# Kernel tuning notes

Hardware: AMD Instinct MI355X
Metric: run time of the kernel (lower is better)

Reference implementation:

```python
import jax, jax.numpy as jnp
import numpy as np

T, B, E, H = 256, 8, 512, 32
EXP = 512            # number of expanded (periodic-image) keys
SMOOTH = 20.0        # smooth_factor


def setup_inputs() -> dict:
    key = jax.random.key(0)
    ks = jax.random.split(key, 12)
    s = 1.0 / np.sqrt(E)
    return {
        "query": jax.random.normal(ks[0], (T, B, E), dtype=jnp.float32),
        "outcell_index": jax.random.randint(ks[1], (B, EXP), 0, T),
        "expand_mask": jax.random.bernoulli(ks[2], 0.1, (B, EXP)),
        "key_padding_mask": jax.random.bernoulli(ks[3], 0.1, (B, T)),
        "local_attention_weight": jax.random.uniform(ks[4], (B, T, T + EXP), dtype=jnp.float32),
        "Wq": jax.random.normal(ks[5], (E, E), dtype=jnp.float32) * s,
        "bq": jnp.zeros((E,), dtype=jnp.float32),
        "Wk": jax.random.normal(ks[6], (E, E), dtype=jnp.float32) * s,   # k_bias=False
        "Wv": jax.random.normal(ks[7], (E, E), dtype=jnp.float32) * s,
        "bv": jnp.zeros((E,), dtype=jnp.float32),
        "Wo": jax.random.normal(ks[8], (E, E), dtype=jnp.float32) * s,
        "bo": jnp.zeros((E,), dtype=jnp.float32),
    }


def reference(query, outcell_index, expand_mask, key_padding_mask,
              local_attention_weight, Wq, bq, Wk, Wv, bv, Wo, bo):
    t, b, e = query.shape
    hd = e // H
    # QKV projections (torch Linear: y = x @ W.T + b)
    q = jnp.einsum('tbe,fe->tbf', query, Wq) + bq
    k = jnp.einsum('tbe,fe->tbf', query, Wk)          # no k bias
    v = jnp.einsum('tbe,fe->tbf', query, Wv) + bv
    # PBC gather-expand K/V along the time axis
    oc = outcell_index.T[:, :, None]                  # [EXP, B, 1]
    k = jnp.concatenate([k, jnp.take_along_axis(k, oc, axis=0)], axis=0)  # [S,B,E]
    v = jnp.concatenate([v, jnp.take_along_axis(v, oc, axis=0)], axis=0)
    s_len = k.shape[0]
    # [len, B, E] -> [B, H, len, hd]
    qh = q.reshape(t, b, H, hd).transpose(1, 2, 0, 3)
    kh = k.reshape(s_len, b, H, hd).transpose(1, 2, 0, 3)
    vh = v.reshape(s_len, b, H, hd).transpose(1, 2, 0, 3)
    # NOTE: forward() never applies self.scaling in this path (faithful)
    scores = jnp.einsum('bhtd,bhsd->bhts', qh, kh)    # [B,H,T,S]
    law = local_attention_weight[:, None]             # [B,1,T,S]
    scores = (scores + SMOOTH) * law - SMOOTH         # smooth softmax
    kpm = jnp.concatenate([key_padding_mask, expand_mask], axis=1)  # [B,S]
    scores = jnp.where(kpm[:, None, None, :], -jnp.inf, scores)
    probs = jax.nn.softmax(scores, axis=-1)
    probs = probs * law                               # post-softmax reweight
    attn = jnp.einsum('bhts,bhsd->bhtd', probs, vh)   # [B,H,T,hd]
    attn = attn.transpose(2, 0, 1, 3).reshape(t, b, e)
    return jnp.einsum('tbe,fe->tbf', attn, Wo) + bo
```

## Files before the change

kernel.cpp:

```cpp
#include <hip/hip_runtime.h>
#include <stdint.h>

#define T_ 256
#define B_ 8
#define E_ 512
#define H_ 32
#define HD_ 16
#define EXP_ 512
#define S_ 768
#define M_ 2048
#define SMOOTH_ 20.0f
#define PSTR 36
#define VSTR 800
#define OSTR 20

typedef __attribute__((ext_vector_type(8)))  short bf16x8;
typedef __attribute__((ext_vector_type(4)))  float f32x4;
typedef __attribute__((ext_vector_type(16))) float f32x16;

__device__ __forceinline__ unsigned int pk2(float a, float b)
{
    unsigned int ua = __float_as_uint(a);
    ua = ua + 0x7FFFu + ((ua >> 16) & 1u);
    unsigned int ub = __float_as_uint(b);
    ub = ub + 0x7FFFu + ((ub >> 16) & 1u);
    return (ua >> 16) | (ub & 0xFFFF0000u);
}
__device__ __forceinline__ ushort bf1(float a)
{
    unsigned int u = __float_as_uint(a);
    u = u + 0x7FFFu + ((u >> 16) & 1u);
    return (ushort)(u >> 16);
}

union U16 { uint4 u; bf16x8 v; };

__global__ __launch_bounds__(256)
void conv_kernel(const float* __restrict__ X,
                 const float* __restrict__ Wq, const float* __restrict__ Wk,
                 const float* __restrict__ Wv, const float* __restrict__ Wo,
                 ushort* __restrict__ Xb, ushort* __restrict__ Wb)
{
    const int seg = blockIdx.x >> 6;
    const int blk = blockIdx.x & 63;
    const float* src;
    ushort* dst;
    if (seg < 4) { src = X + (size_t)seg * 262144; dst = Xb + (size_t)seg * 262144; }
    else {
        const float* ws_[4] = {Wq, Wk, Wv, Wo};
        src = ws_[seg - 4];
        dst = Wb + (size_t)(seg - 4) * 262144;
    }
    const int base = blk * 4096 + threadIdx.x * 16;
    float4 f0 = *(const float4*)&src[base + 0];
    float4 f1 = *(const float4*)&src[base + 4];
    float4 f2 = *(const float4*)&src[base + 8];
    float4 f3 = *(const float4*)&src[base + 12];
    *(uint4*)&dst[base + 0] = make_uint4(pk2(f0.x, f0.y), pk2(f0.z, f0.w),
                                         pk2(f1.x, f1.y), pk2(f1.z, f1.w));
    *(uint4*)&dst[base + 8] = make_uint4(pk2(f2.x, f2.y), pk2(f2.z, f2.w),
                                         pk2(f3.x, f3.y), pk2(f3.z, f3.w));
}

__device__ __forceinline__ void mfma_gemm_body_bf(const ushort* __restrict__ X,
                                                  const ushort* __restrict__ W,
                                                  int m0, int n0,
                                                  f32x4 acc[2][2],
                                                  ushort* As, ushort* Bs)
{
    const int tid  = threadIdx.x;
    const int lrow = tid >> 2;
    const int kq   = tid & 3;
    const int l    = tid & 63;
    const int w    = tid >> 6;
    const int wm   = w & 1;
    const int wn   = w >> 1;
    const int lq   = l >> 4;
    const int ln   = l & 15;

    const ushort* Xr = &X[(size_t)(m0 + lrow) * E_ + kq * 16];
    const ushort* Wr = &W[(size_t)(n0 + lrow) * E_ + kq * 16];
    ushort* Aw = &As[lrow * 72 + kq * 16];
    ushort* Bw = &Bs[lrow * 72 + kq * 16];

    for (int k0 = 0; k0 < E_; k0 += 64) {
        uint4 a0 = *(const uint4*)&Xr[k0 + 0];
        uint4 a1 = *(const uint4*)&Xr[k0 + 8];
        uint4 b0 = *(const uint4*)&Wr[k0 + 0];
        uint4 b1 = *(const uint4*)&Wr[k0 + 8];
        __syncthreads();
        *(uint4*)&Aw[0] = a0;
        *(uint4*)&Aw[8] = a1;
        *(uint4*)&Bw[0] = b0;
        *(uint4*)&Bw[8] = b1;
        __syncthreads();
#pragma unroll
        for (int kb = 0; kb < 2; ++kb) {
            bf16x8 af0 = *(const bf16x8*)&As[(32 * wm + ln) * 72 + 32 * kb + lq * 8];
            bf16x8 af1 = *(const bf16x8*)&As[(32 * wm + 16 + ln) * 72 + 32 * kb + lq * 8];
            bf16x8 bf0 = *(const bf16x8*)&Bs[(32 * wn + ln) * 72 + 32 * kb + lq * 8];
            bf16x8 bf1 = *(const bf16x8*)&Bs[(32 * wn + 16 + ln) * 72 + 32 * kb + lq * 8];
            acc[0][0] = __builtin_amdgcn_mfma_f32_16x16x32_bf16(af0, bf0, acc[0][0], 0, 0, 0);
            acc[0][1] = __builtin_amdgcn_mfma_f32_16x16x32_bf16(af0, bf1, acc[0][1], 0, 0, 0);
            acc[1][0] = __builtin_amdgcn_mfma_f32_16x16x32_bf16(af1, bf0, acc[1][0], 0, 0, 0);
            acc[1][1] = __builtin_amdgcn_mfma_f32_16x16x32_bf16(af1, bf1, acc[1][1], 0, 0, 0);
        }
    }
}

__global__ __launch_bounds__(256)
void qkv_gemm(const ushort* __restrict__ Xb, const ushort* __restrict__ Wb,
              const float* __restrict__ bq, const float* __restrict__ bv,
              ushort* __restrict__ Qb, ushort* __restrict__ Kb,
              ushort* __restrict__ VTb)
{
    __shared__ __align__(16) ushort As[64 * 72];
    __shared__ __align__(16) ushort Bs[64 * 72];
    const int z = blockIdx.z;
    const ushort* W    = Wb + (size_t)z * 262144;
    const float*  bias = (z == 0) ? bq : (z == 2 ? bv : nullptr);

    const int m0 = blockIdx.y * 64;
    const int n0 = blockIdx.x * 64;

    f32x4 acc[2][2];
#pragma unroll
    for (int i = 0; i < 2; ++i)
#pragma unroll
        for (int j = 0; j < 2; ++j)
            acc[i][j] = (f32x4){0.f, 0.f, 0.f, 0.f};

    mfma_gemm_body_bf(Xb, W, m0, n0, acc, As, Bs);

    const int l  = threadIdx.x & 63;
    const int w  = threadIdx.x >> 6;
    const int wm = w & 1;
    const int wn = w >> 1;
    const int lq = l >> 4;
    const int ln = l & 15;

#pragma unroll
    for (int j = 0; j < 2; ++j) {
        const int nb = n0 + 32 * wn + 16 * j;
        const int h  = nb >> 4;
        const int d  = ln;
        const float bv_ = bias ? bias[nb + ln] : 0.f;
#pragma unroll
        for (int i = 0; i < 2; ++i) {
#pragma unroll
            for (int r = 0; r < 4; ++r) {
                const int m = m0 + 32 * wm + 16 * i + lq * 4 + r;
                const int t = m >> 3;
                const int b = m & 7;
                const int bh = b * H_ + h;
                const ushort val = bf1(acc[i][j][r] + bv_);
                if (z == 0)      Qb[((size_t)bh * T_ + t) * HD_ + d] = val;
                else if (z == 1) Kb[((size_t)bh * T_ + t) * HD_ + d] = val;
                else             VTb[((size_t)bh * HD_ + d) * T_ + t] = val;
            }
        }
    }
}

__global__ __launch_bounds__(256)
void out_gemm(const ushort* __restrict__ Ab, const ushort* __restrict__ Wob,
              const float* __restrict__ bo, float* __restrict__ dst)
{
    __shared__ __align__(16) ushort As[64 * 72];
    __shared__ __align__(16) ushort Bs[64 * 72];
    const int m0 = blockIdx.y * 64;
    const int n0 = blockIdx.x * 64;

    f32x4 acc[2][2];
#pragma unroll
    for (int i = 0; i < 2; ++i)
#pragma unroll
        for (int j = 0; j < 2; ++j)
            acc[i][j] = (f32x4){0.f, 0.f, 0.f, 0.f};

    mfma_gemm_body_bf(Ab, Wob, m0, n0, acc, As, Bs);

    const int l  = threadIdx.x & 63;
    const int w  = threadIdx.x >> 6;
    const int wm = w & 1;
    const int wn = w >> 1;
    const int lq = l >> 4;
    const int ln = l & 15;

#pragma unroll
    for (int j = 0; j < 2; ++j) {
        const int nb = n0 + 32 * wn + 16 * j;
        const float bo_ = bo[nb + ln];
#pragma unroll
        for (int i = 0; i < 2; ++i) {
#pragma unroll
            for (int r = 0; r < 4; ++r) {
                const int m = m0 + 32 * wm + 16 * i + lq * 4 + r;
                dst[(size_t)m * E_ + nb + ln] = acc[i][j][r] + bo_;
            }
        }
    }
}

__global__ __launch_bounds__(512)
void attn_kernel(const ushort* __restrict__ Qb, const ushort* __restrict__ Kb,
                 const ushort* __restrict__ VTb, const float* __restrict__ LAW,
                 const int* __restrict__ kpm, const int* __restrict__ em,
                 const int* __restrict__ oc, ushort* __restrict__ Ab)
{
    __shared__ __align__(16) ushort Ks[S_ * HD_];
    __shared__ __align__(16) ushort Vt[HD_ * VSTR];
    __shared__ __align__(16) float  msf[S_];
    __shared__ __align__(16) ushort Pb[8][32 * PSTR];

    float* Obuf = (float*)Ks;
    float* Zb   = (float*)Ks + 128 * OSTR;

    const int tid    = threadIdx.x;
    const int blk    = blockIdx.x;
    const int bh     = blk >> 1;
    const int thalf  = blk & 1;
    const int b      = bh >> 5;
    const int h      = bh & 31;

    ((uint4*)Ks)[tid] = ((const uint4*)&Kb[(size_t)bh * T_ * HD_])[tid];
    {
        const int row = tid >> 5, ch = tid & 31;
        *(uint4*)&Vt[row * VSTR + ch * 8] =
            *(const uint4*)&VTb[((size_t)bh * HD_ + row) * T_ + ch * 8];
    }
    {
        const int j   = tid;
        const int src = oc[b * EXP_ + j];
        const uint4* kr = (const uint4*)&Kb[((size_t)bh * T_ + src) * HD_];
        *(uint4*)&Ks[(T_ + j) * HD_ + 0] = kr[0];
        *(uint4*)&Ks[(T_ + j) * HD_ + 8] = kr[1];
#pragma unroll
        for (int d = 0; d < 16; ++d)
            Vt[d * VSTR + T_ + j] = VTb[((size_t)bh * HD_ + d) * T_ + src];
    }
    {
        const int s = tid;
        const int m = (s < T_) ? kpm[b * T_ + s] : em[b * EXP_ + (s - T_)];
        msf[s] = m ? 0.f : 1.f;
        if (tid < 256) {
            const int s2 = 512 + tid;
            msf[s2] = em[b * EXP_ + (s2 - T_)] ? 0.f : 1.f;
        }
    }

    const int w      = tid >> 6;
    const int l      = tid & 63;
    const int tloc   = l & 31;
    const int khalf  = l >> 5;
    const int wt     = w & 3;
    const int sh     = w >> 2;
    const int tglob  = thalf * 128 + wt * 32 + tloc;
    bf16x8 qf = *(const bf16x8*)&Qb[((size_t)bh * T_ + tglob) * HD_ + khalf * 8];

    __syncthreads();

    const f32x16 zero16 = {0.f,0.f,0.f,0.f,0.f,0.f,0.f,0.f,
                           0.f,0.f,0.f,0.f,0.f,0.f,0.f,0.f};
    f32x4 o0 = {0.f, 0.f, 0.f, 0.f};
    f32x4 o1 = {0.f, 0.f, 0.f, 0.f};
    float Z = 0.f;

    const float* lawp = &LAW[((size_t)b * T_ + tglob) * S_];
    ushort* prow = &Pb[w][tloc * PSTR];
    const int tl = l & 15;
    const int kg = l >> 4;

    for (int i = sh * 12; i < sh * 12 + 12; ++i) {
        bf16x8 kf = *(const bf16x8*)&Ks[(i * 32 + tloc) * HD_ + khalf * 8];
        f32x16 sc = __builtin_amdgcn_mfma_f32_32x32x16_bf16(kf, qf, zero16, 0, 0, 0);

#pragma unroll
        for (int qd = 0; qd < 4; ++qd) {
            const int sb = i * 32 + qd * 8 + khalf * 4;
            float4 mf = *(const float4*)&msf[sb];
            float4 lw = *(const float4*)&lawp[sb];
            float e0, e1, e2, e3;
            {
                float x = (sc[qd*4+0] + SMOOTH_) * lw.x - SMOOTH_;
                e0 = mf.x * __expf(x - 50.f);
                x = (sc[qd*4+1] + SMOOTH_) * lw.y - SMOOTH_;
                e1 = mf.y * __expf(x - 50.f);
                x = (sc[qd*4+2] + SMOOTH_) * lw.z - SMOOTH_;
                e2 = mf.z * __expf(x - 50.f);
                x = (sc[qd*4+3] + SMOOTH_) * lw.w - SMOOTH_;
                e3 = mf.w * __expf(x - 50.f);
            }
            Z += (e0 + e1) + (e2 + e3);
            *(uint2*)&prow[qd * 8 + khalf * 4] =
                make_uint2(pk2(e0 * lw.x, e1 * lw.y), pk2(e2 * lw.z, e3 * lw.w));
        }

        bf16x8 vf = *(const bf16x8*)&Vt[tl * VSTR + i * 32 + kg * 8];
        {
            const ushort* pr0 = &Pb[w][(0 * 16 + tl) * PSTR + kg * 8];
            U16 u;
            uint2 a0 = *(const uint2*)pr0;
            uint2 a1 = *(const uint2*)(pr0 + 4);
            u.u = make_uint4(a0.x, a0.y, a1.x, a1.y);
            o0 = __builtin_amdgcn_mfma_f32_16x16x32_bf16(vf, u.v, o0, 0, 0, 0);
            const ushort* pr1 = &Pb[w][(1 * 16 + tl) * PSTR + kg * 8];
            uint2 b0 = *(const uint2*)pr1;
            uint2 b1 = *(const uint2*)(pr1 + 4);
            u.u = make_uint4(b0.x, b0.y, b1.x, b1.y);
            o1 = __builtin_amdgcn_mfma_f32_16x16x32_bf16(vf, u.v, o1, 0, 0, 0);
        }
    }

    Z += __shfl_xor(Z, 32);

    __syncthreads();

    if (sh == 1) {
#pragma unroll
        for (int th = 0; th < 2; ++th) {
            const f32x4 o = th ? o1 : o0;
            *(float4*)&Obuf[((wt * 2 + th) * 16 + tl) * OSTR + kg * 4] =
                make_float4(o[0], o[1], o[2], o[3]);
        }
        if (l < 32) Zb[wt * 32 + tloc] = Z;
    }
    __syncthreads();

    if (sh == 0) {
        const float Ztot = Z + Zb[wt * 32 + tloc];
#pragma unroll
        for (int th = 0; th < 2; ++th) {
            const float Zt  = __shfl(Ztot, th * 16 + tl);
            const float inv = (Zt > 0.f) ? 1.f / Zt : 0.f;
            float4 po = *(const float4*)&Obuf[((wt * 2 + th) * 16 + tl) * OSTR + kg * 4];
            const f32x4 o = th ? o1 : o0;
            const int t = thalf * 128 + wt * 32 + th * 16 + tl;
            float ov[4] = {o[0] + po.x, o[1] + po.y, o[2] + po.z, o[3] + po.w};
#pragma unroll
            for (int r = 0; r < 4; ++r) {
                const int d = kg * 4 + r;
                Ab[((size_t)t * B_ + b) * E_ + h * HD_ + d] = bf1(ov[r] * inv);
            }
        }
    }
}

extern "C" void kernel_launch(void* const* d_in, const int* in_sizes, int n_in,
                              void* d_out, int out_size, void* d_ws, size_t ws_size,
                              hipStream_t stream)
{
    const float* query = (const float*)d_in[0];
    const int*   oc    = (const int*)d_in[1];
    const int*   em    = (const int*)d_in[2];
    const int*   kpm   = (const int*)d_in[3];
    const float* law   = (const float*)d_in[4];
    const float* Wq    = (const float*)d_in[5];
    const float* bq    = (const float*)d_in[6];
    const float* Wk    = (const float*)d_in[7];
    const float* Wv    = (const float*)d_in[8];
    const float* bv    = (const float*)d_in[9];
    const float* Wo    = (const float*)d_in[10];
    const float* bo    = (const float*)d_in[11];
    float* out = (float*)d_out;

    ushort* Xb  = (ushort*)d_ws;
    ushort* Wb  = Xb  + (size_t)1048576;
    ushort* Qb  = Wb  + (size_t)1048576;
    ushort* Kb  = Qb  + (size_t)1048576;
    ushort* VTb = Kb  + (size_t)1048576;
    ushort* Ab  = VTb + (size_t)1048576;

    conv_kernel<<<512, 256, 0, stream>>>(query, Wq, Wk, Wv, Wo, Xb, Wb);

    dim3 gq(E_ / 64, M_ / 64, 3);
    qkv_gemm<<<gq, 256, 0, stream>>>(Xb, Wb, bq, bv, Qb, Kb, VTb);

    attn_kernel<<<B_ * H_ * 2, 512, 0, stream>>>(Qb, Kb, VTb, law, kpm, em, oc, Ab);

    dim3 go(E_ / 64, M_ / 64, 1);
    out_gemm<<<go, 256, 0, stream>>>(Ab, Wb + (size_t)3 * 262144, bo, out);
}
```

Baseline: 130.5 us.

## Coalesce QKV/attention/output stores via LDS staging and head-major intermediate layout

The QKV GEMM epilogue now stages the bf16 tile in shared memory and writes full 16-element head rows with vector stores. V is kept in the same [bh,t,d] layout as Q and K instead of transposed, and the attention kernel transposes V into LDS itself. Attention output is written head-major through an LDS buffer with 16-byte stores, and the output GEMM reads A directly from that layout. The GEMM main loop also prefetches the next k-slice into registers before the MFMAs. This targets scattered 2-byte global stores, at the cost of extra syncs and scattered LDS writes.

Result: no change. 129.2 us (-1.0%).

```diff
diff --git a/kernel.cpp b/kernel.cpp
--- a/kernel.cpp
+++ b/kernel.cpp
@@ -62,9 +62,10 @@
                                          pk2(f3.x, f3.y), pk2(f3.z, f3.w));
 }
 
-__device__ __forceinline__ void mfma_gemm_body_bf(const ushort* __restrict__ X,
-                                                  const ushort* __restrict__ W,
-                                                  int m0, int n0,
+__device__ __forceinline__ void mfma_gemm_body_bf(const ushort* __restrict__ Xr,
+                                                  int xstep,
+                                                  const ushort* __restrict__ Wr,
+                                                  int wstep,
                                                   f32x4 acc[2][2],
                                                   ushort* As, ushort* Bs)
 {
@@ -78,22 +79,28 @@
     const int lq   = l >> 4;
     const int ln   = l & 15;
 
-    const ushort* Xr = &X[(size_t)(m0 + lrow) * E_ + kq * 16];
-    const ushort* Wr = &W[(size_t)(n0 + lrow) * E_ + kq * 16];
     ushort* Aw = &As[lrow * 72 + kq * 16];
     ushort* Bw = &Bs[lrow * 72 + kq * 16];
 
-    for (int k0 = 0; k0 < E_; k0 += 64) {
-        uint4 a0 = *(const uint4*)&Xr[k0 + 0];
-        uint4 a1 = *(const uint4*)&Xr[k0 + 8];
-        uint4 b0 = *(const uint4*)&Wr[k0 + 0];
-        uint4 b1 = *(const uint4*)&Wr[k0 + 8];
+    uint4 a0 = *(const uint4*)&Xr[0];
+    uint4 a1 = *(const uint4*)&Xr[8];
+    uint4 b0 = *(const uint4*)&Wr[0];
+    uint4 b1 = *(const uint4*)&Wr[8];
+
+    for (int it = 0; it < E_ / 64; ++it) {
         __syncthreads();
         *(uint4*)&Aw[0] = a0;
         *(uint4*)&Aw[8] = a1;
         *(uint4*)&Bw[0] = b0;
         *(uint4*)&Bw[8] = b1;
         __syncthreads();
+        if (it < E_ / 64 - 1) {
+            Xr += xstep; Wr += wstep;
+            a0 = *(const uint4*)&Xr[0];
+            a1 = *(const uint4*)&Xr[8];
+            b0 = *(const uint4*)&Wr[0];
+            b1 = *(const uint4*)&Wr[8];
+        }
 #pragma unroll
         for (int kb = 0; kb < 2; ++kb) {
             bf16x8 af0 = *(const bf16x8*)&As[(32 * wm + ln) * 72 + 32 * kb + lq * 8];
@@ -112,13 +119,16 @@
 void qkv_gemm(const ushort* __restrict__ Xb, const ushort* __restrict__ Wb,
               const float* __restrict__ bq, const float* __restrict__ bv,
               ushort* __restrict__ Qb, ushort* __restrict__ Kb,
-              ushort* __restrict__ VTb)
-{
-    __shared__ __align__(16) ushort As[64 * 72];
-    __shared__ __align__(16) ushort Bs[64 * 72];
+              ushort* __restrict__ Vb)
+{
+    __shared__ __align__(16) ushort AsBs[2 * 64 * 72];
+    ushort* As = AsBs;
+    ushort* Bs = AsBs + 64 * 72;
+
     const int z = blockIdx.z;
     const ushort* W    = Wb + (size_t)z * 262144;
     const float*  bias = (z == 0) ? bq : (z == 2 ? bv : nullptr);
+    ushort* dst        = (z == 0) ? Qb : (z == 1 ? Kb : Vb);
 
     const int m0 = blockIdx.y * 64;
     const int n0 = blockIdx.x * 64;
@@ -130,35 +140,49 @@
         for (int j = 0; j < 2; ++j)
             acc[i][j] = (f32x4){0.f, 0.f, 0.f, 0.f};
 
-    mfma_gemm_body_bf(Xb, W, m0, n0, acc, As, Bs);
-
-    const int l  = threadIdx.x & 63;
-    const int w  = threadIdx.x >> 6;
+    const int tid  = threadIdx.x;
+    const int lrow = tid >> 2;
+    const int kq   = tid & 3;
+    mfma_gemm_body_bf(&Xb[(size_t)(m0 + lrow) * E_ + kq * 16], 64,
+                      &W[(size_t)(n0 + lrow) * E_ + kq * 16], 64,
+                      acc, As, Bs);
+
+    const int l  = tid & 63;
+    const int w  = tid >> 6;
     const int wm = w & 1;
     const int wn = w >> 1;
     const int lq = l >> 4;
     const int ln = l & 15;
 
+    const float b0_ = bias ? bias[n0 + 32 * wn + ln]      : 0.f;
+    const float b1_ = bias ? bias[n0 + 32 * wn + 16 + ln] : 0.f;
+
+    __syncthreads();
+    ushort* Ls = As;
 #pragma unroll
     for (int j = 0; j < 2; ++j) {
-        const int nb = n0 + 32 * wn + 16 * j;
-        const int h  = nb >> 4;
-        const int d  = ln;
-        const float bv_ = bias ? bias[nb + ln] : 0.f;
-#pragma unroll
-        for (int i = 0; i < 2; ++i) {
-#pragma unroll
-            for (int r = 0; r < 4; ++r) {
-                const int m = m0 + 32 * wm + 16 * i + lq * 4 + r;
-                const int t = m >> 3;
-                const int b = m & 7;
-                const int bh = b * H_ + h;
-                const ushort val = bf1(acc[i][j][r] + bv_);
-                if (z == 0)      Qb[((size_t)bh * T_ + t) * HD_ + d] = val;
-                else if (z == 1) Kb[((size_t)bh * T_ + t) * HD_ + d] = val;
-                else             VTb[((size_t)bh * HD_ + d) * T_ + t] = val;
-            }
-        }
+        const float bb = j ? b1_ : b0_;
+#pragma unroll
+        for (int i = 0; i < 2; ++i)
+#pragma unroll
+            for (int r = 0; r < 4; ++r)
+                Ls[(32 * wm + 16 * i + lq * 4 + r) * 72 + 32 * wn + 16 * j + ln] =
+                    bf1(acc[i][j][r] + bb);
+    }
+    __syncthreads();
+
+    {
+        const int lm = tid & 63;
+        const int hh = tid >> 6;
+        uint4 f0 = *(const uint4*)&Ls[lm * 72 + hh * 16];
+        uint4 f1 = *(const uint4*)&Ls[lm * 72 + hh * 16 + 8];
+        const int m = m0 + lm;
+        const int t = m >> 3;
+        const int b = m & 7;
+        const int h = (n0 >> 4) + hh;
+        ushort* dp = &dst[(((size_t)(b * H_ + h)) * T_ + t) * HD_];
+        *(uint4*)&dp[0] = f0;
+        *(uint4*)&dp[8] = f1;
     }
 }
 
@@ -166,8 +190,10 @@
 void out_gemm(const ushort* __restrict__ Ab, const ushort* __restrict__ Wob,
               const float* __restrict__ bo, float* __restrict__ dst)
 {
-    __shared__ __align__(16) ushort As[64 * 72];
-    __shared__ __align__(16) ushort Bs[64 * 72];
+    __shared__ __align__(16) ushort AsBs[2 * 64 * 72];
+    ushort* As = AsBs;
+    ushort* Bs = AsBs + 64 * 72;
+
     const int m0 = blockIdx.y * 64;
     const int n0 = blockIdx.x * 64;
 
@@ -178,33 +204,63 @@
         for (int j = 0; j < 2; ++j)
             acc[i][j] = (f32x4){0.f, 0.f, 0.f, 0.f};
 
-    mfma_gemm_body_bf(Ab, Wob, m0, n0, acc, As, Bs);
-
-    const int l  = threadIdx.x & 63;
-    const int w  = threadIdx.x >> 6;
+    const int tid  = threadIdx.x;
+    const int lrow = tid >> 2;
+    const int kq   = tid & 3;
+    const int m    = m0 + lrow;
+    const int t    = m >> 3;
+    const int b    = m & 7;
+    mfma_gemm_body_bf(&Ab[(((size_t)(b * H_ + kq)) * T_ + t) * HD_], 4 * T_ * HD_,
+                      &Wob[(size_t)(n0 + lrow) * E_ + kq * 16], 64,
+                      acc, As, Bs);
+
+    const int l  = tid & 63;
+    const int w  = tid >> 6;
     const int wm = w & 1;
     const int wn = w >> 1;
     const int lq = l >> 4;
     const int ln = l & 15;
 
+    const float bo0 = bo[n0 + 32 * wn + ln];
+    const float bo1 = bo[n0 + 32 * wn + 16 + ln];
+
+    __syncthreads();
+    float* Lf = (float*)AsBs;
 #pragma unroll
     for (int j = 0; j < 2; ++j) {
-        const int nb = n0 + 32 * wn + 16 * j;
-        const float bo_ = bo[nb + ln];
-#pragma unroll
-        for (int i = 0; i < 2; ++i) {
-#pragma unroll
-            for (int r = 0; r < 4; ++r) {
-                const int m = m0 + 32 * wm + 16 * i + lq * 4 + r;
-                dst[(size_t)m * E_ + nb + ln] = acc[i][j][r] + bo_;
-            }
-        }
-    }
+        const float bb = j ? bo1 : bo0;
+#pragma unroll
+        for (int i = 0; i < 2; ++i)
+#pragma unroll
+            for (int r = 0; r < 4; ++r)
+                Lf[(32 * wm + 16 * i + lq * 4 + r) * 68 + 32 * wn + 16 * j + ln] =
+                    acc[i][j][r] + bb;
+    }
+    __syncthreads();
+
+    {
+        const int lm = tid & 63;
+        const int hh = tid >> 6;
+        float* dp = &dst[(size_t)(m0 + lm) * E_ + n0 + hh * 16];
+#pragma unroll
+        for (int c = 0; c < 4; ++c) {
+            float4 v = *(const float4*)&Lf[lm * 68 + hh * 16 + c * 4];
+            *(float4*)&dp[c * 4] = v;
+        }
+    }
+}
+
+__device__ __forceinline__ void scat8(ushort* d, uint4 u)
+{
+    d[0 * VSTR] = (ushort)(u.x);  d[1 * VSTR] = (ushort)(u.x >> 16);
+    d[2 * VSTR] = (ushort)(u.y);  d[3 * VSTR] = (ushort)(u.y >> 16);
+    d[4 * VSTR] = (ushort)(u.z);  d[5 * VSTR] = (ushort)(u.z >> 16);
+    d[6 * VSTR] = (ushort)(u.w);  d[7 * VSTR] = (ushort)(u.w >> 16);
 }
 
 __global__ __launch_bounds__(512)
 void attn_kernel(const ushort* __restrict__ Qb, const ushort* __restrict__ Kb,
-                 const ushort* __restrict__ VTb, const float* __restrict__ LAW,
+                 const ushort* __restrict__ Vb, const float* __restrict__ LAW,
                  const int* __restrict__ kpm, const int* __restrict__ em,
                  const int* __restrict__ oc, ushort* __restrict__ Ab)
 {
@@ -215,6 +271,7 @@
 
     float* Obuf = (float*)Ks;
     float* Zb   = (float*)Ks + 128 * OSTR;
+    ushort* Ob  = (ushort*)Pb;
 
     const int tid    = threadIdx.x;
     const int blk    = blockIdx.x;
@@ -225,9 +282,10 @@
 
     ((uint4*)Ks)[tid] = ((const uint4*)&Kb[(size_t)bh * T_ * HD_])[tid];
     {
-        const int row = tid >> 5, ch = tid & 31;
-        *(uint4*)&Vt[row * VSTR + ch * 8] =
-            *(const uint4*)&VTb[((size_t)bh * HD_ + row) * T_ + ch * 8];
+        const int t    = tid >> 1;
+        const int half = tid & 1;
+        uint4 v = *(const uint4*)&Vb[((size_t)bh * T_ + t) * HD_ + half * 8];
+        scat8(&Vt[half * 8 * VSTR + t], v);
     }
     {
         const int j   = tid;
@@ -235,9 +293,9 @@
         const uint4* kr = (const uint4*)&Kb[((size_t)bh * T_ + src) * HD_];
         *(uint4*)&Ks[(T_ + j) * HD_ + 0] = kr[0];
         *(uint4*)&Ks[(T_ + j) * HD_ + 8] = kr[1];
-#pragma unroll
-        for (int d = 0; d < 16; ++d)
-            Vt[d * VSTR + T_ + j] = VTb[((size_t)bh * HD_ + d) * T_ + src];
+        const uint4* vr = (const uint4*)&Vb[((size_t)bh * T_ + src) * HD_];
+        scat8(&Vt[T_ + j], vr[0]);
+        scat8(&Vt[8 * VSTR + T_ + j], vr[1]);
     }
     {
         const int s = tid;
@@ -335,14 +393,18 @@
             const float inv = (Zt > 0.f) ? 1.f / Zt : 0.f;
             float4 po = *(const float4*)&Obuf[((wt * 2 + th) * 16 + tl) * OSTR + kg * 4];
             const f32x4 o = th ? o1 : o0;
-            const int t = thalf * 128 + wt * 32 + th * 16 + tl;
-            float ov[4] = {o[0] + po.x, o[1] + po.y, o[2] + po.z, o[3] + po.w};
-#pragma unroll
-            for (int r = 0; r < 4; ++r) {
-                const int d = kg * 4 + r;
-                Ab[((size_t)t * B_ + b) * E_ + h * HD_ + d] = bf1(ov[r] * inv);
-            }
-        }
+            const int trow = wt * 32 + th * 16 + tl;
+            float ov[4] = {(o[0] + po.x) * inv, (o[1] + po.y) * inv,
+                           (o[2] + po.z) * inv, (o[3] + po.w) * inv};
+            *(uint*)&Ob[trow * 16 + kg * 4]     = pk2(ov[0], ov[1]);
+            *(uint*)&Ob[trow * 16 + kg * 4 + 2] = pk2(ov[2], ov[3]);
+        }
+    }
+    __syncthreads();
+
+    if (tid < 256) {
+        ushort* dp = &Ab[(((size_t)(b * H_ + h)) * T_ + thalf * 128) * HD_];
+        *(uint4*)&dp[tid * 8] = *(const uint4*)&Ob[tid * 8];
     }
 }
 
@@ -368,15 +430,15 @@
     ushort* Wb  = Xb  + (size_t)1048576;
     ushort* Qb  = Wb  + (size_t)1048576;
     ushort* Kb  = Qb  + (size_t)1048576;
-    ushort* VTb = Kb  + (size_t)1048576;
-    ushort* Ab  = VTb + (size_t)1048576;
+    ushort* Vb  = Kb  + (size_t)1048576;
+    ushort* Ab  = Vb  + (size_t)1048576;
 
     conv_kernel<<<512, 256, 0, stream>>>(query, Wq, Wk, Wv, Wo, Xb, Wb);
 
     dim3 gq(E_ / 64, M_ / 64, 3);
-    qkv_gemm<<<gq, 256, 0, stream>>>(Xb, Wb, bq, bv, Qb, Kb, VTb);
-
-    attn_kernel<<<B_ * H_ * 2, 512, 0, stream>>>(Qb, Kb, VTb, law, kpm, em, oc, Ab);
+    qkv_gemm<<<gq, 256, 0, stream>>>(Xb, Wb, bq, bv, Qb, Kb, Vb);
+
+    attn_kernel<<<B_ * H_ * 2, 512, 0, stream>>>(Qb, Kb, Vb, law, kpm, em, oc, Ab);
 
     dim3 go(E_ / 64, M_ / 64, 1);
     out_gemm<<<go, 256, 0, stream>>>(Ab, Wb + (size_t)3 * 262144, bo, out);
```
